# Performance work log

Measured on AMD Instinct MI355X. Metric: run time of the kernel, lower is better.

Reference implementation:

```python
import jax, jax.numpy as jnp
import numpy as np

DIM = 768
N_HEADS = 12
HEAD_DIM = DIM // N_HEADS
B, S = 2, 2048


def fibonacci_mask(seq_len, causal=True):
    fibs = [1, 1]
    while fibs[-1] + fibs[-2] <= seq_len:
        fibs.append(fibs[-1] + fibs[-2])
    mask = np.zeros((seq_len, seq_len), dtype=bool)
    i = np.arange(seq_len)
    mask[i, i] = True  # self
    for f in fibs:
        rows = i[i - f >= 0]
        mask[rows, rows - f] = True
        if not causal:
            rows = i[i + f < seq_len]
            mask[rows, rows + f] = True
    return mask


def setup_inputs() -> dict:
    key = jax.random.key(0)
    k1, k2, k3, k4, k5 = jax.random.split(key, 5)
    x = jax.random.normal(k1, (B, S, DIM), dtype=jnp.float32)
    # Linear weights (torch layout: [out, in]), small init
    w_qkv = jax.random.normal(k2, (3 * DIM, DIM), dtype=jnp.float32) * (DIM ** -0.5)
    b_qkv = jax.random.normal(k3, (3 * DIM,), dtype=jnp.float32) * 0.02
    w_out = jax.random.normal(k4, (DIM, DIM), dtype=jnp.float32) * (DIM ** -0.5)
    b_out = jax.random.normal(k5, (DIM,), dtype=jnp.float32) * 0.02
    mask = jnp.asarray(fibonacci_mask(S, causal=True))  # [S,S] bool constant
    return {"x": x, "w_qkv": w_qkv, "b_qkv": b_qkv, "w_out": w_out, "b_out": b_out, "mask": mask}


def reference(x, w_qkv, b_qkv, w_out, b_out, mask):
    Bx, Sx, D = x.shape
    qkv = x @ w_qkv.T + b_qkv                                   # [B,S,3D]
    qkv = qkv.reshape(Bx, Sx, 3, N_HEADS, HEAD_DIM)
    qkv = jnp.transpose(qkv, (2, 0, 3, 1, 4))                   # [3,B,H,S,hd]
    q, k, v = qkv[0], qkv[1], qkv[2]
    scale = HEAD_DIM ** -0.5
    attn = jnp.einsum('bhqd,bhkd->bhqk', q, k) * scale          # [B,H,S,S]
    attn = jnp.where(mask[None, None], attn, -jnp.inf)
    attn = jax.nn.softmax(attn, axis=-1)
    attn = jnp.nan_to_num(attn, nan=0.0)
    out = jnp.einsum('bhqk,bhkd->bhqd', attn, v)                # [B,H,S,hd]
    out = jnp.transpose(out, (0, 2, 1, 3)).reshape(Bx, Sx, D)
    return out @ w_out.T + b_out
```

## Files before the change

kernel.cpp:

```cpp
#include <hip/hip_runtime.h>
#include <hip/hip_bf16.h>

#define DIM   768
#define NH    12
#define HD    64
#define BB    2
#define SS    2048
#define QKVN  (3 * DIM)
#define MM    (BB * SS)

typedef __attribute__((ext_vector_type(8))) short bf16x8;
typedef __attribute__((ext_vector_type(8))) short short8;
typedef __attribute__((ext_vector_type(4))) float f32x4;

__device__ __forceinline__ short f2bf(float f) {
    unsigned int u = __float_as_uint(f);
    unsigned int r = (u + 0x7FFFu + ((u >> 16) & 1u)) >> 16;
    return (short)r;
}
__device__ __forceinline__ float bf2f(short s) {
    return __uint_as_float((unsigned int)(unsigned short)s << 16);
}

__device__ __forceinline__ void gld16(const short* g, short* l) {
    __builtin_amdgcn_global_load_lds(
        (const __attribute__((address_space(1))) void*)g,
        (__attribute__((address_space(3))) void*)l, 16, 0, 0);
}

__global__ __launch_bounds__(256) void conv_kernel(
    const float* __restrict__ x,  short* __restrict__ xb,
    const float* __restrict__ wq, short* __restrict__ wqb,
    const float* __restrict__ wo, short* __restrict__ wob)
{
    const int nx = (MM * DIM) / 8;
    const int nq = (QKVN * DIM) / 8;
    int i8 = blockIdx.x * 256 + threadIdx.x;
    const float* src; short* dst;
    if (i8 < nx)           { src = x;  dst = xb; }
    else if (i8 < nx + nq) { i8 -= nx; src = wq; dst = wqb; }
    else                   { i8 -= nx + nq; src = wo; dst = wob; }
    const float4* p = (const float4*)src + (size_t)i8 * 2;
    float4 a = p[0], b = p[1];
    short8 r;
    r[0] = f2bf(a.x); r[1] = f2bf(a.y); r[2] = f2bf(a.z); r[3] = f2bf(a.w);
    r[4] = f2bf(b.x); r[5] = f2bf(b.y); r[6] = f2bf(b.z); r[7] = f2bf(b.w);
    *((short8*)dst + i8) = r;
}


template<int RT>
__device__ __forceinline__ void stage_op(const short* gb, int K, int k0, short* ld)
{
#pragma unroll
    for (int ii = 0; ii < RT / 64; ++ii)
        gld16(gb + (size_t)(64 * ii) * K + k0, ld + ii * 4096);
}

template<int MF, int NF>
__device__ __forceinline__ void compute_tile(
    const short* lsA, const short* lsB, int arow, int brow, int kg, int sw,
    f32x4 acc[MF][NF])
{
#pragma unroll
    for (int kk = 0; kk < 2; ++kk) {
        const int ko = (kk * 32 + kg * 8) ^ sw;
        bf16x8 af[MF], bfr[NF];
#pragma unroll
        for (int i = 0; i < MF; ++i)
            af[i] = *(const bf16x8*)&lsA[(arow + i * 16) * 64 + ko];
#pragma unroll
        for (int j = 0; j < NF; ++j)
            bfr[j] = *(const bf16x8*)&lsB[(brow + j * 16) * 64 + ko];
#pragma unroll
        for (int i = 0; i < MF; ++i)
#pragma unroll
            for (int j = 0; j < NF; ++j)
                acc[i][j] = __builtin_amdgcn_mfma_f32_16x16x32_bf16(
                    af[i], bfr[j], acc[i][j], 0, 0, 0);
    }
}

__global__ __launch_bounds__(512) void gemm_qkv_kernel(
    const short* __restrict__ A, const short* __restrict__ Bm,
    const float* __restrict__ bias, short* __restrict__ qkvh)
{
    constexpr int K = DIM;
    __shared__ short lsA0[8192], lsB0[8192], lsA1[8192], lsB1[8192];

    const int t    = threadIdx.x;
    const int lane = t & 63;
    const int wid  = t >> 6;
    const int wrow = wid >> 2, wcol = wid & 3;
    const int l16  = lane & 15;
    const int kg   = lane >> 4;
    const int row0 = blockIdx.y * 128;
    const int col0 = blockIdx.x * 128;

    const int srow = t >> 3;
    const int scol = ((t & 7) ^ (srow & 7)) * 8;
    const short* Ab = A  + (size_t)(row0 + srow) * K + scol;
    const short* Bb = Bm + (size_t)(col0 + srow) * K + scol;
    short* ldA0 = lsA0 + t * 8;  short* ldB0 = lsB0 + t * 8;
    short* ldA1 = lsA1 + t * 8;  short* ldB1 = lsB1 + t * 8;
    const int arow = wrow * 64 + l16;
    const int brow = wcol * 32 + l16;
    const int sw   = (l16 & 7) * 8;

    f32x4 acc[4][2];
#pragma unroll
    for (int i = 0; i < 4; ++i)
#pragma unroll
        for (int j = 0; j < 2; ++j) acc[i][j] = (f32x4){0.f, 0.f, 0.f, 0.f};

    constexpr int NT = K / 64;
    stage_op<128>(Ab, K, 0, ldA0);
    stage_op<128>(Bb, K, 0, ldB0);
    __syncthreads();
    for (int kt = 0; kt < NT; kt += 2) {
        stage_op<128>(Ab, K, (kt + 1) * 64, ldA1);
        stage_op<128>(Bb, K, (kt + 1) * 64, ldB1);
        compute_tile<4, 2>(lsA0, lsB0, arow, brow, kg, sw, acc);
        __syncthreads();
        if (kt + 2 < NT) {
            stage_op<128>(Ab, K, (kt + 2) * 64, ldA0);
            stage_op<128>(Bb, K, (kt + 2) * 64, ldB0);
        }
        compute_tile<4, 2>(lsA1, lsB1, arow, brow, kg, sw, acc);
        __syncthreads();
    }

#pragma unroll
    for (int j = 0; j < 2; ++j) {
        const int col = col0 + wcol * 32 + j * 16 + l16;
        const int ty = col / DIM;
        const int hh = (col % DIM) >> 6;
        const int dd = col & 63;
        const float bv = bias[col];
        const size_t cbase = ((size_t)(ty * BB * NH) * SS) * HD;
#pragma unroll
        for (int i = 0; i < 4; ++i) {
            const int rbase = row0 + wrow * 64 + i * 16 + kg * 4;
#pragma unroll
            for (int r = 0; r < 4; ++r) {
                const int row = rbase + r;
                const int bq = row >> 11, sq = row & 2047;
                qkvh[cbase + (((size_t)(bq * NH + hh) * SS + sq) << 6) + dd] =
                    f2bf(acc[i][j][r] + bv);
            }
        }
    }
}

__global__ __launch_bounds__(512) void gemm_out_kernel(
    const short* __restrict__ A, const short* __restrict__ Bm,
    const float* __restrict__ bias, float* __restrict__ C)
{
    constexpr int K = DIM, N = DIM;
    __shared__ short lsA0[4096], lsB0[8192], lsA1[4096], lsB1[8192];

    const int t    = threadIdx.x;
    const int lane = t & 63;
    const int wid  = t >> 6;
    const int wrow = wid >> 2, wcol = wid & 3;
    const int l16  = lane & 15;
    const int kg   = lane >> 4;
    const int row0 = blockIdx.y * 64;
    const int col0 = blockIdx.x * 128;

    const int srow = t >> 3;
    const int scol = ((t & 7) ^ (srow & 7)) * 8;
    const short* Ab = A  + (size_t)(row0 + srow) * K + scol;
    const short* Bb = Bm + (size_t)(col0 + srow) * K + scol;
    short* ldA0 = lsA0 + t * 8;  short* ldB0 = lsB0 + t * 8;
    short* ldA1 = lsA1 + t * 8;  short* ldB1 = lsB1 + t * 8;
    const int arow = wrow * 32 + l16;
    const int brow = wcol * 32 + l16;
    const int sw   = (l16 & 7) * 8;

    f32x4 acc[2][2];
#pragma unroll
    for (int i = 0; i < 2; ++i)
#pragma unroll
        for (int j = 0; j < 2; ++j) acc[i][j] = (f32x4){0.f, 0.f, 0.f, 0.f};

    constexpr int NT = K / 64;
    stage_op<64>(Ab, K, 0, ldA0);
    stage_op<128>(Bb, K, 0, ldB0);
    __syncthreads();
    for (int kt = 0; kt < NT; kt += 2) {
        stage_op<64>(Ab, K, (kt + 1) * 64, ldA1);
        stage_op<128>(Bb, K, (kt + 1) * 64, ldB1);
        compute_tile<2, 2>(lsA0, lsB0, arow, brow, kg, sw, acc);
        __syncthreads();
        if (kt + 2 < NT) {
            stage_op<64>(Ab, K, (kt + 2) * 64, ldA0);
            stage_op<128>(Bb, K, (kt + 2) * 64, ldB0);
        }
        compute_tile<2, 2>(lsA1, lsB1, arow, brow, kg, sw, acc);
        __syncthreads();
    }

#pragma unroll
    for (int j = 0; j < 2; ++j) {
        const int col = col0 + wcol * 32 + j * 16 + l16;
        const float bv = bias[col];
#pragma unroll
        for (int i = 0; i < 2; ++i) {
            const int rbase = row0 + wrow * 32 + i * 16 + kg * 4;
#pragma unroll
            for (int r = 0; r < 4; ++r)
                C[(size_t)(rbase + r) * N + col] = acc[i][j][r] + bv;
        }
    }
}

__global__ __launch_bounds__(256) void fib_attn_kernel(
    const short* __restrict__ qkvh, short* __restrict__ attn)
{
    const int idx   = blockIdx.x;
    const int j     = idx >> 3;
    const int bh    = (idx & 7) + 8 * (j >> 6);
    const int chunk = j & 63;
    const int wid   = threadIdx.x >> 6;
    const int lane  = threadIdx.x & 63;
    const int ql    = lane >> 3;
    const int c     = lane & 7;
    const int s     = chunk * 32 + wid * 8 + ql;
    const int b = bh / NH, h = bh % NH;

    constexpr size_t TYB = (size_t)BB * NH * SS * HD;
    const size_t base = ((size_t)bh * SS) << 6;
    const short* Kp = qkvh + TYB + base;
    const short* Vp = qkvh + 2 * TYB + base;

    float qv[8];
    {
        bf16x8 v = *(const bf16x8*)(qkvh + base + ((size_t)s << 6) + c * 8);
#pragma unroll
        for (int e = 0; e < 8; ++e) qv[e] = bf2f(v[e]);
    }

    constexpr int NF = 17;
    const int fib[NF] = {0, 1, 2, 3, 5, 8, 13, 21, 34, 55, 89, 144,
                         233, 377, 610, 987, 1597};
    float sc[NF];
#pragma unroll
    for (int f = 0; f < NF; ++f) {
        const bool ok = (fib[f] <= s);
        const int sk = ok ? s - fib[f] : s;
        bf16x8 kv = *(const bf16x8*)(Kp + ((size_t)sk << 6) + c * 8);
        float part = 0.f;
#pragma unroll
        for (int e = 0; e < 8; ++e) part += qv[e] * bf2f(kv[e]);
        part += __shfl_xor(part, 1, 64);
        part += __shfl_xor(part, 2, 64);
        part += __shfl_xor(part, 4, 64);
        sc[f] = ok ? part * 0.125f : -1e30f;
    }

    float mx = sc[0];
#pragma unroll
    for (int f = 1; f < NF; ++f) mx = fmaxf(mx, sc[f]);
    float den = 0.f;
#pragma unroll
    for (int f = 0; f < NF; ++f) { sc[f] = __expf(sc[f] - mx); den += sc[f]; }

    float o[8];
#pragma unroll
    for (int e = 0; e < 8; ++e) o[e] = 0.f;
#pragma unroll
    for (int f = 0; f < NF; ++f) {
        const int sk = (fib[f] <= s) ? s - fib[f] : s;
        bf16x8 vv = *(const bf16x8*)(Vp + ((size_t)sk << 6) + c * 8);
        const float w = sc[f];
#pragma unroll
        for (int e = 0; e < 8; ++e) o[e] += w * bf2f(vv[e]);
    }

    const float inv = 1.f / den;
    short8 r;
#pragma unroll
    for (int e = 0; e < 8; ++e) r[e] = f2bf(o[e] * inv);
    *(short8*)(attn + (size_t)(b * SS + s) * DIM + h * HD + c * 8) = r;
}

extern "C" void kernel_launch(void* const* d_in, const int* in_sizes, int n_in,
                              void* d_out, int out_size, void* d_ws, size_t ws_size,
                              hipStream_t stream)
{
    const float* x     = (const float*)d_in[0];
    const float* w_qkv = (const float*)d_in[1];
    const float* b_qkv = (const float*)d_in[2];
    const float* w_out = (const float*)d_in[3];
    const float* b_out = (const float*)d_in[4];
    float* out = (float*)d_out;

    short* qkvh  = (short*)d_ws;
    short* attnb = (short*)((char*)d_ws + 18874368);
    short* xb    = (short*)((char*)d_ws + 25165824);
    short* wqkvb = (short*)((char*)d_ws + 31457280);
    short* woutb = (short*)((char*)d_ws + 34996224);

    conv_kernel<<<dim3(2688, 1, 1), dim3(256, 1, 1), 0, stream>>>(
        x, xb, w_qkv, wqkvb, w_out, woutb);

    gemm_qkv_kernel<<<dim3(QKVN / 128, MM / 128, 1), dim3(512, 1, 1), 0, stream>>>(
        xb, wqkvb, b_qkv, qkvh);

    fib_attn_kernel<<<dim3(1536, 1, 1), dim3(256, 1, 1), 0, stream>>>(qkvh, attnb);

    gemm_out_kernel<<<dim3(DIM / 128, MM / 64, 1), dim3(512, 1, 1), 0, stream>>>(
        attnb, woutb, b_out, out);
}
```

Baseline: 69.26 us.

## Restructure GEMM K-loop pipeline with two-ahead prefetch and explicit vmcnt waits

Both projection GEMMs now prefetch two K tiles before the loop and keep a distance-two prefetch in steady state. Each phase reads all LDS fragments into registers, waits on lgkmcnt and barriers, issues the next global-to-LDS loads, runs the MFMAs, then waits with a partial vmcnt so only the older tile must have arrived. This replaces full __syncthreads with finer-grained waits to overlap global loads with compute. It adds register pressure from holding both k-halves of fragments, and correctness depends on hand-counted vmcnt values.

```diff
diff --git a/kernel.cpp b/kernel.cpp
--- a/kernel.cpp
+++ b/kernel.cpp
@@ -26,6 +26,12 @@
     __builtin_amdgcn_global_load_lds(
         (const __attribute__((address_space(1))) void*)g,
         (__attribute__((address_space(3))) void*)l, 16, 0, 0);
+}
+
+template<int N> __device__ __forceinline__ void waitvm() {
+    if constexpr (N == 0) asm volatile("s_waitcnt vmcnt(0)" ::: "memory");
+    else if constexpr (N == 3) asm volatile("s_waitcnt vmcnt(3)" ::: "memory");
+    else if constexpr (N == 4) asm volatile("s_waitcnt vmcnt(4)" ::: "memory");
 }
 
 __global__ __launch_bounds__(256) void conv_kernel(
@@ -58,34 +64,58 @@
 }
 
 template<int MF, int NF>
-__device__ __forceinline__ void compute_tile(
+__device__ __forceinline__ void read_frags(
     const short* lsA, const short* lsB, int arow, int brow, int kg, int sw,
-    f32x4 acc[MF][NF])
+    bf16x8 af[2][MF], bf16x8 bfr[2][NF])
 {
 #pragma unroll
     for (int kk = 0; kk < 2; ++kk) {
         const int ko = (kk * 32 + kg * 8) ^ sw;
-        bf16x8 af[MF], bfr[NF];
 #pragma unroll
         for (int i = 0; i < MF; ++i)
-            af[i] = *(const bf16x8*)&lsA[(arow + i * 16) * 64 + ko];
+            af[kk][i] = *(const bf16x8*)&lsA[(arow + i * 16) * 64 + ko];
 #pragma unroll
         for (int j = 0; j < NF; ++j)
-            bfr[j] = *(const bf16x8*)&lsB[(brow + j * 16) * 64 + ko];
+            bfr[kk][j] = *(const bf16x8*)&lsB[(brow + j * 16) * 64 + ko];
+    }
+}
+
+template<int MF, int NF>
+__device__ __forceinline__ void mfma_frags(
+    bf16x8 af[2][MF], bf16x8 bfr[2][NF], f32x4 acc[MF][NF])
+{
+#pragma unroll
+    for (int kk = 0; kk < 2; ++kk)
 #pragma unroll
         for (int i = 0; i < MF; ++i)
 #pragma unroll
             for (int j = 0; j < NF; ++j)
                 acc[i][j] = __builtin_amdgcn_mfma_f32_16x16x32_bf16(
-                    af[i], bfr[j], acc[i][j], 0, 0, 0);
-    }
+                    af[kk][i], bfr[kk][j], acc[i][j], 0, 0, 0);
+}
+
+template<int MF, int NF, int ART, int BRT, int VC>
+__device__ __forceinline__ void phase_steady(
+    const short* lsA, const short* lsB, short* ldA, short* ldB,
+    const short* Ab, const short* Bb, int K, int knext,
+    int arow, int brow, int kg, int sw, f32x4 acc[MF][NF])
+{
+    bf16x8 af[2][MF], bfr[2][NF];
+    read_frags<MF, NF>(lsA, lsB, arow, brow, kg, sw, af, bfr);
+    asm volatile("s_waitcnt lgkmcnt(0)" ::: "memory");
+    __builtin_amdgcn_s_barrier();
+    stage_op<ART>(Ab, K, knext, ldA);
+    stage_op<BRT>(Bb, K, knext, ldB);
+    mfma_frags<MF, NF>(af, bfr, acc);
+    waitvm<VC>();
+    __builtin_amdgcn_s_barrier();
 }
 
 __global__ __launch_bounds__(512) void gemm_qkv_kernel(
     const short* __restrict__ A, const short* __restrict__ Bm,
     const float* __restrict__ bias, short* __restrict__ qkvh)
 {
-    constexpr int K = DIM;
+    constexpr int K = DIM, NT = 12;
     __shared__ short lsA0[8192], lsB0[8192], lsA1[8192], lsB1[8192];
 
     const int t    = threadIdx.x;
@@ -113,21 +143,28 @@
 #pragma unroll
         for (int j = 0; j < 2; ++j) acc[i][j] = (f32x4){0.f, 0.f, 0.f, 0.f};
 
-    constexpr int NT = K / 64;
     stage_op<128>(Ab, K, 0, ldA0);
     stage_op<128>(Bb, K, 0, ldB0);
-    __syncthreads();
-    for (int kt = 0; kt < NT; kt += 2) {
-        stage_op<128>(Ab, K, (kt + 1) * 64, ldA1);
-        stage_op<128>(Bb, K, (kt + 1) * 64, ldB1);
-        compute_tile<4, 2>(lsA0, lsB0, arow, brow, kg, sw, acc);
-        __syncthreads();
-        if (kt + 2 < NT) {
-            stage_op<128>(Ab, K, (kt + 2) * 64, ldA0);
-            stage_op<128>(Bb, K, (kt + 2) * 64, ldB0);
-        }
-        compute_tile<4, 2>(lsA1, lsB1, arow, brow, kg, sw, acc);
-        __syncthreads();
+    stage_op<128>(Ab, K, 64, ldA1);
+    stage_op<128>(Bb, K, 64, ldB1);
+    waitvm<4>();
+    __builtin_amdgcn_s_barrier();
+
+#pragma unroll
+    for (int kt = 0; kt < NT - 2; kt += 2) {
+        phase_steady<4, 2, 128, 128, 4>(lsA0, lsB0, ldA0, ldB0, Ab, Bb, K,
+                                        (kt + 2) * 64, arow, brow, kg, sw, acc);
+        phase_steady<4, 2, 128, 128, 4>(lsA1, lsB1, ldA1, ldB1, Ab, Bb, K,
+                                        (kt + 3) * 64, arow, brow, kg, sw, acc);
+    }
+    {
+        bf16x8 af[2][4], bfr[2][2];
+        read_frags<4, 2>(lsA0, lsB0, arow, brow, kg, sw, af, bfr);
+        mfma_frags<4, 2>(af, bfr, acc);
+        waitvm<0>();
+        __builtin_amdgcn_s_barrier();
+        read_frags<4, 2>(lsA1, lsB1, arow, brow, kg, sw, af, bfr);
+        mfma_frags<4, 2>(af, bfr, acc);
     }
 
 #pragma unroll
@@ -156,7 +193,7 @@
     const short* __restrict__ A, const short* __restrict__ Bm,
     const float* __restrict__ bias, float* __restrict__ C)
 {
-    constexpr int K = DIM, N = DIM;
+    constexpr int K = DIM, N = DIM, NT = 12;
     __shared__ short lsA0[4096], lsB0[8192], lsA1[4096], lsB1[8192];
 
     const int t    = threadIdx.x;
@@ -184,21 +221,28 @@
 #pragma unroll
         for (int j = 0; j < 2; ++j) acc[i][j] = (f32x4){0.f, 0.f, 0.f, 0.f};
 
-    constexpr int NT = K / 64;
     stage_op<64>(Ab, K, 0, ldA0);
     stage_op<128>(Bb, K, 0, ldB0);
-    __syncthreads();
-    for (int kt = 0; kt < NT; kt += 2) {
-        stage_op<64>(Ab, K, (kt + 1) * 64, ldA1);
-        stage_op<128>(Bb, K, (kt + 1) * 64, ldB1);
-        compute_tile<2, 2>(lsA0, lsB0, arow, brow, kg, sw, acc);
-        __syncthreads();
-        if (kt + 2 < NT) {
-            stage_op<64>(Ab, K, (kt + 2) * 64, ldA0);
-            stage_op<128>(Bb, K, (kt + 2) * 64, ldB0);
-        }
-        compute_tile<2, 2>(lsA1, lsB1, arow, brow, kg, sw, acc);
-        __syncthreads();
+    stage_op<64>(Ab, K, 64, ldA1);
+    stage_op<128>(Bb, K, 64, ldB1);
+    waitvm<3>();
+    __builtin_amdgcn_s_barrier();
+
+#pragma unroll
+    for (int kt = 0; kt < NT - 2; kt += 2) {
+        phase_steady<2, 2, 64, 128, 3>(lsA0, lsB0, ldA0, ldB0, Ab, Bb, K,
+                                       (kt + 2) * 64, arow, brow, kg, sw, acc);
+        phase_steady<2, 2, 64, 128, 3>(lsA1, lsB1, ldA1, ldB1, Ab, Bb, K,
+                                       (kt + 3) * 64, arow, brow, kg, sw, acc);
+    }
+    {
+        bf16x8 af[2][2], bfr[2][2];
+        read_frags<2, 2>(lsA0, lsB0, arow, brow, kg, sw, af, bfr);
+        mfma_frags<2, 2>(af, bfr, acc);
+        waitvm<0>();
+        __builtin_amdgcn_s_barrier();
+        read_frags<2, 2>(lsA1, lsB1, arow, brow, kg, sw, af, bfr);
+        mfma_frags<2, 2>(af, bfr, acc);
     }
 
 #pragma unroll
```

Measured after the change: 59.47 us. 1.16x faster.
